# Kernel tuning notes

Measured on AMD Instinct MI355X. Metric: run time of the kernel, lower is better.

## Reference

```python
import jax, jax.numpy as jnp
import numpy as np
from jax import lax

DT = 0.1  # forward() default dt


def setup_inputs() -> dict:
    key = jax.random.key(0)
    k1, k2, k3 = jax.random.split(key, 3)
    B, S = 256, 65536
    strain = jax.random.normal(k1, (B, S), dtype=jnp.float32)
    strain_rate = jax.random.normal(k2, (B, S), dtype=jnp.float32)
    log_E = jnp.zeros((1,), dtype=jnp.float32)            # E = 1.0
    log_eta = jnp.log(jnp.full((1,), 10.0, jnp.float32))  # eta = 10.0
    return {"strain": strain, "strain_rate": strain_rate,
            "log_E": log_E, "log_eta": log_eta}


def reference(strain, strain_rate, log_E, log_eta):
    # Maxwell element: stress[0] = E*strain[0] + eta*rate[0]
    #                  stress[t] = a*stress[t-1] + E*(strain[t]-strain[t-1]),  a = exp(-dt/tau)
    E = jnp.exp(log_E)          # (1,)
    eta = jnp.exp(log_eta)      # (1,)
    tau = eta / E
    a = jnp.exp(-DT / tau)      # (1,) constant decay

    B, S = strain.shape
    # driving term u[t]
    u0 = E * strain[:, :1] + eta * strain_rate[:, :1]          # (B,1)
    u_rest = E * (strain[:, 1:] - strain[:, :-1])              # (B,S-1)
    u = jnp.concatenate([u0, u_rest], axis=1)                  # (B,S)
    # decay coeffs: first step has no history
    A = jnp.concatenate([jnp.ones((B, 1), strain.dtype),
                         jnp.broadcast_to(a, (B, S - 1))], axis=1)

    def combine(x, y):
        a1, b1 = x
        a2, b2 = y
        return a1 * a2, b2 + a2 * b1

    _, stress = lax.associative_scan(combine, (A, u), axis=1)  # (B,S)
    return stress
```

## Files before the change

kernel.cpp:

```cpp
#include <hip/hip_runtime.h>
#include <math.h>


#define DT_F  0.1f
#define S_LEN 65536
#define B_ROWS 256
#define CHUNK 1024
#define WARM  512
#define WPB   4
#define CPR   (S_LEN / CHUNK)
#define BPR   (CPR / WPB)

typedef float nfloat4 __attribute__((ext_vector_type(4)));

template<int CTRL, int RM>
__device__ __forceinline__ float dpp0(float x) {
    return __int_as_float(__builtin_amdgcn_update_dpp(
        0, __float_as_int(x), CTRL, RM, 0xF, false));
}
template<int N>
__device__ __forceinline__ float dpp_shr(float x) { return dpp0<0x110 + N, 0xF>(x); }
__device__ __forceinline__ float bcast15(float x) { return dpp0<0x142, 0xA>(x); }
__device__ __forceinline__ float bcast31(float x) { return dpp0<0x143, 0xC>(x); }
__device__ __forceinline__ float wshr1(float x)   { return dpp0<0x138, 0xF>(x); }
__device__ __forceinline__ float rdl(float x, int l) {
    return __int_as_float(__builtin_amdgcn_readlane(__float_as_int(x), l));
}

__global__ __launch_bounds__(256) void maxwell_scan(
    const float* __restrict__ strain,
    const float* __restrict__ rate,
    const float* __restrict__ log_E,
    const float* __restrict__ log_eta,
    float* __restrict__ out)
{
    __shared__ float Tlds[WPB * 4];
    __shared__ float S0lds;

    const int lane = threadIdx.x & 63;
    const int wv   = threadIdx.x >> 6;
    const int row  = blockIdx.x / BPR;
    const int cb   = (blockIdx.x % BPR) * WPB;
    const int c    = cb + wv;

    const float E   = __expf(log_E[0]);
    const float eta = __expf(log_eta[0]);
    const float lam = -DT_F * E / eta;
    const float a   = __expf(lam);
    const float a2 = a * a, a3 = a2 * a, a4 = a2 * a2, a8 = a4 * a4;
    const float a16 = a8 * a8, a32 = a16 * a16, a64 = a32 * a32;
    const float a128 = a64 * a64, a256 = a128 * a128;
    const float a512 = a256 * a256, a768 = a512 * a256, a1024 = a512 * a512;
    const float cc = E * (a - 1.0f);
    const float cca1 = cc * a, cca2 = cc * a2, cca3 = cc * a3;

    const int  lrow = lane & 15;
    const float alane = __expf(lam * (float)(4 * lane));
    const float wX    = __expf(lam * (float)(4 * lrow));
    const float wm1   = wX * a4;
    const float wm2   = (lane >= 48) ? wm1 * a64 : wm1;

    const int rowbase = row * S_LEN;
    const int t0 = c * CHUNK;
    const nfloat4* s4 = (const nfloat4*)(strain + rowbase);
    nfloat4*       o4 = (nfloat4*)(out + rowbase);

    nfloat4 w0, w1;
    const bool do_warm = (wv == 0) && (cb != 0);
    if (do_warm) {
        const int vw = ((t0 - WARM) >> 2) + lane;
        w0 = s4[vw]; w1 = s4[vw + 64];
    }
    const int vp = (t0 >> 2) + lane;
    nfloat4 p0 = s4[vp +   0], p1 = s4[vp +  64], p2 = s4[vp + 128], p3 = s4[vp + 192];

    float etar0 = 0.0f;
    if (c == 0) etar0 = eta * rate[rowbase];

    auto scanW = [&](float fl3) -> float {
        float D = fl3, v;
        v = dpp_shr<1>(D); D = fmaf(a4,  v, D);
        v = dpp_shr<2>(D); D = fmaf(a8,  v, D);
        v = dpp_shr<4>(D); D = fmaf(a16, v, D);
        v = dpp_shr<8>(D); D = fmaf(a32, v, D);
        v = bcast15(D);    D = fmaf(wm1, v, D);
        v = bcast31(D);    D = fmaf(wm2, v, D);
        return D;
    };
    auto groupW = [&](nfloat4 pf) -> float {
        float fl = pf.x;
        fl = fmaf(a, fl, pf.y); fl = fmaf(a, fl, pf.z); fl = fmaf(a, fl, pf.w);
        return scanW(fl);
    };

    float W0 = groupW(p0), W1 = groupW(p1), W2 = groupW(p2), W3 = groupW(p3);
    if (lane == 63) {
        Tlds[wv * 4 + 0] = W0; Tlds[wv * 4 + 1] = W1;
        Tlds[wv * 4 + 2] = W2; Tlds[wv * 4 + 3] = W3;
    }
    float S0 = 0.0f;
    if (do_warm) {
        float Tw0 = rdl(groupW(w0), 63);
        float Tw1 = rdl(groupW(w1), 63);
        S0 = fmaf(a256, Tw0, Tw1);
    }
    if (threadIdx.x == 0) S0lds = S0;
    __syncthreads();

    float S = S0lds;
    for (int j = 0; j < wv; ++j) {
        float Tc = Tlds[j * 4 + 0];
        Tc = fmaf(a256, Tc, Tlds[j * 4 + 1]);
        Tc = fmaf(a256, Tc, Tlds[j * 4 + 2]);
        Tc = fmaf(a256, Tc, Tlds[j * 4 + 3]);
        S = fmaf(a1024, S, Tc);
    }
    const float T0 = Tlds[wv * 4 + 0], T1 = Tlds[wv * 4 + 1], T2 = Tlds[wv * 4 + 2];
    const float Sg0 = S;
    const float Sg1 = fmaf(a256, Sg0, T0);
    const float Sg2 = fmaf(a256, Sg1, T1);
    const float Sg3 = fmaf(a256, Sg2, T2);

    const float rl0 = etar0 * alane;
    const float rl1 = rl0 * a, rl2 = rl0 * a2, rl3 = rl0 * a3;

    auto outg = [&](nfloat4 pf, float W, float Sg, float bse, int vo) {
        float fl0 = pf.x;
        float fl1 = fmaf(a, fl0, pf.y);
        float fl2 = fmaf(a, fl1, pf.z);
        float X  = wshr1(W);
        float Xs = fmaf(alane, Sg, X);
        nfloat4 o;
        o.x = fmaf(cc,   Xs, E * pf.x);
        o.y = fmaf(cca1, Xs, fmaf(cc, fl0, E * pf.y));
        o.z = fmaf(cca2, Xs, fmaf(cc, fl1, E * pf.z));
        o.w = fmaf(cca3, Xs, fmaf(cc, fl2, E * pf.w));
        o.x = fmaf(bse, rl0, o.x);
        o.y = fmaf(bse, rl1, o.y);
        o.z = fmaf(bse, rl2, o.z);
        o.w = fmaf(bse, rl3, o.w);
        o4[vo] = o;
    };
    outg(p0, W0, Sg0, 1.0f, vp +   0);
    outg(p1, W1, Sg1, a256, vp +  64);
    outg(p2, W2, Sg2, a512, vp + 128);
    outg(p3, W3, Sg3, a768, vp + 192);
}

extern "C" void kernel_launch(void* const* d_in, const int* in_sizes, int n_in,
                              void* d_out, int out_size, void* d_ws, size_t ws_size,
                              hipStream_t stream) {
    const float* strain  = (const float*)d_in[0];
    const float* rate    = (const float*)d_in[1];
    const float* log_E   = (const float*)d_in[2];
    const float* log_eta = (const float*)d_in[3];
    float* out = (float*)d_out;

    const int blocks = B_ROWS * BPR;
    maxwell_scan<<<blocks, 256, 0, stream>>>(strain, rate, log_E, log_eta, out);
}
```

Measured before the change: 156.2 us.

## Split each block's span into two sequential halves and overlap compute with stores

Each wave now handles two 512-element chunks in two phases. The second phase is seeded by the first phase's end state, so the warm-up recomputation is paid once per 4096 elements instead of once per 4096 as before, but with half the per-block span logic changed. A custom barrier waits only on LDS counters, so outstanding global loads and stores are not drained at each sync. First-half outputs can be written while second-half scans proceed. The cost is an extra barrier and a serial dependency between the halves. The rate term is handled via a per-wave exp offset.

```diff
diff --git a/kernel.cpp b/kernel.cpp
--- a/kernel.cpp
+++ b/kernel.cpp
@@ -5,11 +5,12 @@
 #define DT_F  0.1f
 #define S_LEN 65536
 #define B_ROWS 256
-#define CHUNK 1024
+#define CHUNK 512
 #define WARM  512
 #define WPB   4
-#define CPR   (S_LEN / CHUNK)
-#define BPR   (CPR / WPB)
+#define SPAN  (CHUNK * WPB)
+#define BSPAN (SPAN * 2)
+#define BPR   (S_LEN / BSPAN)
 
 typedef float nfloat4 __attribute__((ext_vector_type(4)));
 
@@ -27,6 +28,14 @@
     return __int_as_float(__builtin_amdgcn_readlane(__float_as_int(x), l));
 }
 
+__device__ __forceinline__ void sync_lds_keep_vmem() {
+    asm volatile("s_waitcnt lgkmcnt(0)" ::: "memory");
+    __builtin_amdgcn_sched_barrier(0);
+    __builtin_amdgcn_s_barrier();
+    __builtin_amdgcn_sched_barrier(0);
+    asm volatile("" ::: "memory");
+}
+
 __global__ __launch_bounds__(256) void maxwell_scan(
     const float* __restrict__ strain,
     const float* __restrict__ rate,
@@ -34,14 +43,15 @@
     const float* __restrict__ log_eta,
     float* __restrict__ out)
 {
-    __shared__ float Tlds[WPB * 4];
+    __shared__ float T0lds[WPB][2];
+    __shared__ float T1lds[WPB][2];
     __shared__ float S0lds;
+    __shared__ float Sendlds;
 
     const int lane = threadIdx.x & 63;
     const int wv   = threadIdx.x >> 6;
     const int row  = blockIdx.x / BPR;
-    const int cb   = (blockIdx.x % BPR) * WPB;
-    const int c    = cb + wv;
+    const int off  = (blockIdx.x % BPR) * BSPAN;
 
     const float E   = __expf(log_E[0]);
     const float eta = __expf(log_eta[0]);
@@ -49,33 +59,33 @@
     const float a   = __expf(lam);
     const float a2 = a * a, a3 = a2 * a, a4 = a2 * a2, a8 = a4 * a4;
     const float a16 = a8 * a8, a32 = a16 * a16, a64 = a32 * a32;
-    const float a128 = a64 * a64, a256 = a128 * a128;
-    const float a512 = a256 * a256, a768 = a512 * a256, a1024 = a512 * a512;
+    const float a256 = a64 * a64 * a64 * a64;
+    const float a512 = a256 * a256;
     const float cc = E * (a - 1.0f);
     const float cca1 = cc * a, cca2 = cc * a2, cca3 = cc * a3;
 
-    const int  lrow = lane & 15;
     const float alane = __expf(lam * (float)(4 * lane));
-    const float wX    = __expf(lam * (float)(4 * lrow));
+    const float wX    = __expf(lam * (float)(4 * (lane & 15)));
     const float wm1   = wX * a4;
     const float wm2   = (lane >= 48) ? wm1 * a64 : wm1;
 
     const int rowbase = row * S_LEN;
-    const int t0 = c * CHUNK;
     const nfloat4* s4 = (const nfloat4*)(strain + rowbase);
     nfloat4*       o4 = (nfloat4*)(out + rowbase);
 
     nfloat4 w0, w1;
-    const bool do_warm = (wv == 0) && (cb != 0);
+    const bool do_warm = (wv == 0) && (off != 0);
     if (do_warm) {
-        const int vw = ((t0 - WARM) >> 2) + lane;
+        const int vw = ((off - WARM) >> 2) + lane;
         w0 = s4[vw]; w1 = s4[vw + 64];
     }
-    const int vp = (t0 >> 2) + lane;
-    nfloat4 p0 = s4[vp +   0], p1 = s4[vp +  64], p2 = s4[vp + 128], p3 = s4[vp + 192];
+    const int vp0 = (off >> 2) + wv * (CHUNK / 4) + lane;
+    const int vp1 = vp0 + (SPAN / 4);
+    nfloat4 p00 = s4[vp0], p01 = s4[vp0 + 64];
+    nfloat4 p10 = s4[vp1], p11 = s4[vp1 + 64];
 
     float etar0 = 0.0f;
-    if (c == 0) etar0 = eta * rate[rowbase];
+    if (off == 0) etar0 = eta * rate[rowbase];
 
     auto scanW = [&](float fl3) -> float {
         float D = fl3, v;
@@ -93,36 +103,34 @@
         return scanW(fl);
     };
 
-    float W0 = groupW(p0), W1 = groupW(p1), W2 = groupW(p2), W3 = groupW(p3);
-    if (lane == 63) {
-        Tlds[wv * 4 + 0] = W0; Tlds[wv * 4 + 1] = W1;
-        Tlds[wv * 4 + 2] = W2; Tlds[wv * 4 + 3] = W3;
+    float W00 = groupW(p00), W01 = groupW(p01);
+    if (lane == 63) { T0lds[wv][0] = W00; T0lds[wv][1] = W01; }
+    if (wv == 0) {
+        float S0 = 0.0f;
+        if (off != 0) {
+            float Tw0 = rdl(groupW(w0), 63);
+            float Tw1 = rdl(groupW(w1), 63);
+            S0 = fmaf(a256, Tw0, Tw1);
+        }
+        if (lane == 0) S0lds = S0;
     }
-    float S0 = 0.0f;
-    if (do_warm) {
-        float Tw0 = rdl(groupW(w0), 63);
-        float Tw1 = rdl(groupW(w1), 63);
-        S0 = fmaf(a256, Tw0, Tw1);
-    }
-    if (threadIdx.x == 0) S0lds = S0;
-    __syncthreads();
+    sync_lds_keep_vmem();
 
     float S = S0lds;
     for (int j = 0; j < wv; ++j) {
-        float Tc = Tlds[j * 4 + 0];
-        Tc = fmaf(a256, Tc, Tlds[j * 4 + 1]);
-        Tc = fmaf(a256, Tc, Tlds[j * 4 + 2]);
-        Tc = fmaf(a256, Tc, Tlds[j * 4 + 3]);
-        S = fmaf(a1024, S, Tc);
+        float Tc = fmaf(a256, T0lds[j][0], T0lds[j][1]);
+        S = fmaf(a512, S, Tc);
     }
-    const float T0 = Tlds[wv * 4 + 0], T1 = Tlds[wv * 4 + 1], T2 = Tlds[wv * 4 + 2];
     const float Sg0 = S;
-    const float Sg1 = fmaf(a256, Sg0, T0);
-    const float Sg2 = fmaf(a256, Sg1, T1);
-    const float Sg3 = fmaf(a256, Sg2, T2);
+    const float Sg1 = fmaf(a256, Sg0, T0lds[wv][0]);
+    if (wv == WPB - 1) {
+        float Send = fmaf(a256, Sg1, T0lds[WPB - 1][1]);
+        if (lane == 0) Sendlds = Send;
+    }
 
     const float rl0 = etar0 * alane;
     const float rl1 = rl0 * a, rl2 = rl0 * a2, rl3 = rl0 * a3;
+    const float rb0 = __expf(lam * (float)(CHUNK * wv));
 
     auto outg = [&](nfloat4 pf, float W, float Sg, float bse, int vo) {
         float fl0 = pf.x;
@@ -141,10 +149,22 @@
         o.w = fmaf(bse, rl3, o.w);
         o4[vo] = o;
     };
-    outg(p0, W0, Sg0, 1.0f, vp +   0);
-    outg(p1, W1, Sg1, a256, vp +  64);
-    outg(p2, W2, Sg2, a512, vp + 128);
-    outg(p3, W3, Sg3, a768, vp + 192);
+    outg(p00, W00, Sg0, rb0,        vp0);
+    outg(p01, W01, Sg1, rb0 * a256, vp0 + 64);
+
+    float W10 = groupW(p10), W11 = groupW(p11);
+    if (lane == 63) { T1lds[wv][0] = W10; T1lds[wv][1] = W11; }
+    sync_lds_keep_vmem();
+
+    float S2 = Sendlds;
+    for (int j = 0; j < wv; ++j) {
+        float Tc = fmaf(a256, T1lds[j][0], T1lds[j][1]);
+        S2 = fmaf(a512, S2, Tc);
+    }
+    const float Sh0 = S2;
+    const float Sh1 = fmaf(a256, Sh0, T1lds[wv][0]);
+    outg(p10, W10, Sh0, 0.0f, vp1);
+    outg(p11, W11, Sh1, 0.0f, vp1 + 64);
 }
 
 extern "C" void kernel_launch(void* const* d_in, const int* in_sizes, int n_in,
```

Result: no change. 156.7 us (+0.3%).
